# Performance work log

Hardware: AMD Instinct MI355X
Metric: run time of the kernel (lower is better)

Reference implementation:

```python
import jax, jax.numpy as jnp
import numpy as np
import math

H = 2048; NH = 16; HD = 128; E = 8; K = 2; F = 8192; CAP_F = 1.25
B = 2; S = 2048

def _layernorm(x, scale, bias, eps=1e-5):
    m = jnp.mean(x, axis=-1, keepdims=True)
    v = jnp.var(x, axis=-1, keepdims=True)
    return (x - m) * jax.lax.rsqrt(v + eps) * scale + bias

def _rope(x):
    # x: [B, S, NH, HD]; half-split RoPE, theta=10000
    hd = x.shape[-1]
    pos = jnp.arange(x.shape[1], dtype=jnp.float32)
    freqs = 1.0 / (10000.0 ** (jnp.arange(0, hd // 2, dtype=jnp.float32) / (hd // 2)))
    ang = pos[:, None] * freqs[None, :]              # [S, HD/2]
    cos = jnp.cos(ang)[None, :, None, :]
    sin = jnp.sin(ang)[None, :, None, :]
    x1, x2 = jnp.split(x, 2, axis=-1)
    return jnp.concatenate([x1 * cos - x2 * sin, x1 * sin + x2 * cos], axis=-1)

def setup_inputs() -> dict:
    key = jax.random.key(0)
    ks = jax.random.split(key, 16)
    std = 0.02
    inp = {
        'hidden_states': jax.random.normal(ks[0], (B, S, H), jnp.float32),
        'attention_mask': jnp.ones((B, S), jnp.int32),
        'ln1_scale': jnp.ones((H,), jnp.float32), 'ln1_bias': jnp.zeros((H,), jnp.float32),
        'ln2_scale': jnp.ones((H,), jnp.float32), 'ln2_bias': jnp.zeros((H,), jnp.float32),
        'Wq': jax.random.normal(ks[1], (H, NH * HD), jnp.float32) * std,
        'Wk': jax.random.normal(ks[2], (H, NH * HD), jnp.float32) * std,
        'Wv': jax.random.normal(ks[3], (H, NH * HD), jnp.float32) * std,
        'Wo': jax.random.normal(ks[4], (NH * HD, H), jnp.float32) * std,
        'Wg': jax.random.normal(ks[5], (H, H), jnp.float32) * std,
        'bg': jnp.zeros((H,), jnp.float32),
        'ls_attn': jnp.full((H,), 0.1, jnp.float32),
        'ls_moe': jnp.full((H,), 0.1, jnp.float32),
        'router_w': jax.random.normal(ks[6], (H, E), jnp.float32) * std,
        'W1': jax.random.normal(ks[7], (E, H, F), jnp.float32) * std,
        'b1': jnp.zeros((E, F), jnp.float32),
        'W2': jax.random.normal(ks[8], (E, F, H), jnp.float32) * std,
        'b2': jnp.zeros((E, H), jnp.float32),
    }
    return inp

def _forward(hidden_states, attention_mask, ln1_scale, ln1_bias, ln2_scale, ln2_bias,
             Wq, Wk, Wv, Wo, Wg, bg, ls_attn, ls_moe, router_w, W1, b1, W2, b2):
    b, s, h = hidden_states.shape
    # ---- pre-norm MLA attention + residual ----
    xn = _layernorm(hidden_states, ln1_scale, ln1_bias)
    q = (xn @ Wq).reshape(b, s, NH, HD)
    k = (xn @ Wk).reshape(b, s, NH, HD)
    v = (xn @ Wv).reshape(b, s, NH, HD)
    q = _rope(q); k = _rope(k)
    scores = jnp.einsum('bqhd,bkhd->bhqk', q, k) / math.sqrt(HD)
    causal = jnp.tril(jnp.ones((s, s), bool))
    mask = causal[None, None, :, :] & (attention_mask[:, None, None, :] > 0)
    scores = jnp.where(mask, scores, -1e9)
    attn = jax.nn.softmax(scores, axis=-1)
    ctx = jnp.einsum('bhqk,bkhd->bqhd', attn, v).reshape(b, s, NH * HD)
    attn_out = ctx @ Wo
    attn_out = attn_out * jax.nn.sigmoid(xn @ Wg + bg)   # output gating
    attn_out = attn_out * ls_attn                         # layer scale
    hidden_states = hidden_states + attn_out
    # ---- pre-norm MoE FFN + residual ----
    xn2 = _layernorm(hidden_states, ln2_scale, ln2_bias)
    T = b * s
    x = xn2.reshape(T, h)
    logits = (x @ router_w).astype(jnp.float32)           # [T, E]
    probs = jax.nn.softmax(logits, axis=-1)
    gates, idx = jax.lax.top_k(probs, K)                  # [T, K]
    gates = gates / jnp.sum(gates, axis=-1, keepdims=True)
    cap = int(math.ceil(T * K / E * CAP_F))               # expert capacity
    e_flat = idx.reshape(T * K)
    g_flat = gates.reshape(T * K)
    oh = jax.nn.one_hot(e_flat, E, dtype=jnp.int32)       # [TK, E]
    pos = jnp.sum(jnp.cumsum(oh, axis=0) * oh, axis=-1) - 1
    keep = (pos < cap).astype(x.dtype)
    pos_c = jnp.clip(pos, 0, cap - 1)
    x_rep = jnp.repeat(x, K, axis=0)                      # [TK, H]
    buf = jnp.zeros((E, cap, h), x.dtype).at[e_flat, pos_c].add(x_rep * keep[:, None])
    hmid = jax.nn.gelu(jnp.einsum('ech,ehf->ecf', buf, W1) + b1[:, None, :])
    obuf = jnp.einsum('ecf,efh->ech', hmid, W2) + b2[:, None, :]
    tok = obuf[e_flat, pos_c] * (keep * g_flat)[:, None]  # [TK, H]
    moe_out = tok.reshape(T, K, h).sum(axis=1).reshape(b, s, h)
    moe_out = moe_out * ls_moe
    return hidden_states + moe_out

def reference(hidden_states, attention_mask, ln1_scale, ln1_bias, ln2_scale, ln2_bias,
              Wq, Wk, Wv, Wo, Wg, bg, ls_attn, ls_moe, router_w, W1, b1, W2, b2):
    return _forward(hidden_states, attention_mask, ln1_scale, ln1_bias, ln2_scale, ln2_bias,
                    Wq, Wk, Wv, Wo, Wg, bg, ls_attn, ls_moe, router_w, W1, b1, W2, b2)
```

## Files before the change

### kernel.cpp

```cpp
#include <hip/hip_runtime.h>
#include <hip/hip_fp16.h>

typedef _Float16 f16;
typedef _Float16 half8 __attribute__((ext_vector_type(8)));
typedef float floatx4 __attribute__((ext_vector_type(4)));

constexpr int kH  = 2048;
constexpr int kS  = 2048;
constexpr int kB  = 2;
constexpr int kT  = kB * kS;
constexpr int kNH = 16;
constexpr int kHD = 128;
constexpr int kE  = 8;
constexpr int kF  = 8192;
constexpr int kCAP = 1280;
constexpr int kTK = kT * 2;

__device__ __forceinline__ void gload16(const void* g, void* lds_) {
  __builtin_amdgcn_global_load_lds((const __attribute__((address_space(1))) void*)g,
                                   (__attribute__((address_space(3))) void*)lds_,
                                   16, 0, 0);
}

__global__ __launch_bounds__(256) void transpose_cvt(
    const float* __restrict__ src, f16* __restrict__ dst,
    int ldS, int ldD, long sZ, long dZ)
{
  __shared__ float tile[64][65];
  src += (long)blockIdx.z * sZ;
  dst += (long)blockIdx.z * dZ;
  const int kb = blockIdx.y * 64, nb = blockIdx.x * 64;
  const int tx = threadIdx.x & 15, ty = threadIdx.x >> 4;
#pragma unroll
  for (int i = 0; i < 4; i++) {
    const int r = ty + i * 16;
    const float4 v = *(const float4*)&src[(long)(kb + r) * ldS + nb + tx * 4];
    tile[r][tx * 4 + 0] = v.x; tile[r][tx * 4 + 1] = v.y;
    tile[r][tx * 4 + 2] = v.z; tile[r][tx * 4 + 3] = v.w;
  }
  __syncthreads();
#pragma unroll
  for (int i = 0; i < 4; i++) {
    const int n = ty + i * 16;
    union { f16 h[4]; unsigned long long u; } pk;
#pragma unroll
    for (int j = 0; j < 4; j++) pk.h[j] = (f16)tile[tx * 4 + j][n];
    *(unsigned long long*)&dst[(long)(nb + n) * ldD + kb + tx * 4] = pk.u;
  }
}

__global__ __launch_bounds__(256) void ln_kernel(
    const float* __restrict__ x, const float* __restrict__ sc,
    const float* __restrict__ bi, f16* __restrict__ o16, float* __restrict__ o32)
{
  const long row = blockIdx.x;
  const float* xr = x + row * kH;
  const int t = threadIdx.x;
  const float4 u = ((const float4*)xr)[t * 2];
  const float4 v = ((const float4*)xr)[t * 2 + 1];
  float s = u.x + u.y + u.z + u.w + v.x + v.y + v.z + v.w;
  float q = u.x*u.x + u.y*u.y + u.z*u.z + u.w*u.w + v.x*v.x + v.y*v.y + v.z*v.z + v.w*v.w;
#pragma unroll
  for (int m = 1; m < 64; m <<= 1) { s += __shfl_xor(s, m); q += __shfl_xor(q, m); }
  __shared__ float red_s[4], red_q[4];
  const int w = t >> 6, l = t & 63;
  if (l == 0) { red_s[w] = s; red_q[w] = q; }
  __syncthreads();
  s = red_s[0] + red_s[1] + red_s[2] + red_s[3];
  q = red_q[0] + red_q[1] + red_q[2] + red_q[3];
  const float mean = s * (1.f / kH);
  const float var = q * (1.f / kH) - mean * mean;
  const float rstd = rsqrtf(var + 1e-5f);
  const int c = t * 8;
  const float vals[8] = {u.x, u.y, u.z, u.w, v.x, v.y, v.z, v.w};
#pragma unroll
  for (int j = 0; j < 8; j++) {
    const float y = (vals[j] - mean) * rstd * sc[c + j] + bi[c + j];
    o16[row * kH + c + j] = (f16)y;
    if (o32 != nullptr) o32[row * kH + c + j] = y;
  }
}

template <int EPI>
__global__ __launch_bounds__(256) void gemm_kernel(
    const f16* __restrict__ A, const f16* __restrict__ B, void* __restrict__ Cv,
    const float* __restrict__ bias, const int* __restrict__ rowCount,
    int M, int N, int K, long aZ, long bZ, long cZ, long biasZ)
{
  const int z = blockIdx.z;
  if (rowCount != nullptr && (int)(blockIdx.y * 128) >= rowCount[z]) return;
  __shared__ f16 As[128 * 64];
  __shared__ f16 Bs[128 * 64];
  A += (long)z * aZ;  B += (long)z * bZ;
  const int tid = threadIdx.x, w = tid >> 6, l = tid & 63;
  const int g = l >> 4, lr = l & 15;
  const long m0 = (long)blockIdx.y * 128, n0 = (long)blockIdx.x * 128;
  const int wm = (w >> 1) * 64, wn = (w & 1) * 64;
  floatx4 acc[4][4];
#pragma unroll
  for (int i = 0; i < 4; i++)
#pragma unroll
    for (int j = 0; j < 4; j++) acc[i][j] = floatx4{0.f, 0.f, 0.f, 0.f};
  const int lrow = l >> 3, lwb = (l & 7) * 16;
  const int nk = K >> 6;
  for (int kt = 0; kt < nk; kt++) {
    const long k0 = (long)kt * 64;
#pragma unroll
    for (int c = 0; c < 4; c++) {
      const int rbase = w * 32 + c * 8;
      const int row = rbase + lrow;
      const int srcoff = (lwb ^ ((row & 7) << 4)) >> 1;
      gload16(A + (m0 + row) * K + k0 + srcoff, As + rbase * 64);
      gload16(B + (n0 + row) * K + k0 + srcoff, Bs + rbase * 64);
    }
    asm volatile("s_waitcnt vmcnt(0)" ::: "memory");
    __syncthreads();
#pragma unroll
    for (int kc = 0; kc < 2; kc++) {
      half8 af[4], bf[4];
#pragma unroll
      for (int i = 0; i < 4; i++) {
        const int ra = wm + i * 16 + lr;
        af[i] = *(const half8*)((const char*)As + ra * 128 + ((kc * 64 + g * 16) ^ ((ra & 7) << 4)));
        const int rb = wn + i * 16 + lr;
        bf[i] = *(const half8*)((const char*)Bs + rb * 128 + ((kc * 64 + g * 16) ^ ((rb & 7) << 4)));
      }
#pragma unroll
      for (int mi = 0; mi < 4; mi++)
#pragma unroll
        for (int ni = 0; ni < 4; ni++)
          acc[mi][ni] = __builtin_amdgcn_mfma_f32_16x16x32_f16(af[mi], bf[ni], acc[mi][ni], 0, 0, 0);
    }
    __syncthreads();
  }
  const long crow = m0 + wm + g * 4;
  const long ccol = n0 + wn + lr;
#pragma unroll
  for (int mi = 0; mi < 4; mi++)
#pragma unroll
    for (int ni = 0; ni < 4; ni++)
#pragma unroll
      for (int j = 0; j < 4; j++) {
        const long r = crow + mi * 16 + j;
        const long c = ccol + ni * 16;
        float v = acc[mi][ni][j];
        if (EPI == 0) {
          ((float*)Cv)[(long)z * cZ + r * N + c] = v;
        } else {
          v += bias[(long)z * biasZ + c];
          ((f16*)Cv)[(long)z * cZ + r * N + c] = (f16)v;
        }
      }
}

#define STG(SRC, TILE, KC, PAR, MAT) { \
  const f16* s_ = (SRC) + (long)(TILE) * 64 + (KC) * 32; \
  char* d_ = lds + ((PAR) * 65536 + (MAT) * 32768 + (KC) * 16384) + ldsW; \
  gload16(s_, d_); \
  gload16(s_ + 128 * Kl, d_ + 8192); }

#define MROW(MH, MM, AF) \
  acc[(MH)*4+(MM)][0] = __builtin_amdgcn_mfma_f32_16x16x32_f16(AF, bf0, acc[(MH)*4+(MM)][0], 0, 0, 0); \
  acc[(MH)*4+(MM)][1] = __builtin_amdgcn_mfma_f32_16x16x32_f16(AF, bf1, acc[(MH)*4+(MM)][1], 0, 0, 0); \
  acc[(MH)*4+(MM)][2] = __builtin_amdgcn_mfma_f32_16x16x32_f16(AF, bf2, acc[(MH)*4+(MM)][2], 0, 0, 0); \
  acc[(MH)*4+(MM)][3] = __builtin_amdgcn_mfma_f32_16x16x32_f16(AF, bf3, acc[(MH)*4+(MM)][3], 0, 0, 0);

#define PH(PAR, KC, MH, RB, STAGE_STMT, VM_STMT) { \
  const char* au_ = lds + ((PAR) * 65536 + (KC) * 16384); \
  const char* bu_ = lds + ((PAR) * 65536 + 32768 + (KC) * 16384); \
  af0 = *(const half8*)(au_ + afoff + (MH) * 4096 +    0); \
  af1 = *(const half8*)(au_ + afoff + (MH) * 4096 + 1024); \
  af2 = *(const half8*)(au_ + afoff + (MH) * 4096 + 2048); \
  af3 = *(const half8*)(au_ + afoff + (MH) * 4096 + 3072); \
  if (RB) { \
    bf0 = *(const half8*)(bu_ + bfoff +    0); \
    bf1 = *(const half8*)(bu_ + bfoff + 1024); \
    bf2 = *(const half8*)(bu_ + bfoff + 2048); \
    bf3 = *(const half8*)(bu_ + bfoff + 3072); \
  } \
  STAGE_STMT; \
  VM_STMT; \
  __builtin_amdgcn_sched_barrier(0); \
  __builtin_amdgcn_s_barrier(); \
  asm volatile("s_waitcnt lgkmcnt(0)" ::: "memory"); \
  __builtin_amdgcn_sched_barrier(0); \
  __builtin_amdgcn_s_setprio(1); \
  MROW(MH, 0, af0) MROW(MH, 1, af1) MROW(MH, 2, af2) MROW(MH, 3, af3) \
  __builtin_amdgcn_s_setprio(0); \
  __builtin_amdgcn_sched_barrier(0); \
  __builtin_amdgcn_s_barrier(); }

#define VM6 asm volatile("s_waitcnt vmcnt(6)" ::: "memory")
#define VM0 asm volatile("s_waitcnt vmcnt(0)" ::: "memory")
#define NOP (void)0

template <int EPI>
__global__ __launch_bounds__(512, 2) void gemm8p_kernel(
    const f16* __restrict__ A, const f16* __restrict__ B, void* __restrict__ Cv,
    const float* __restrict__ bias, const int* __restrict__ rowCount,
    int M, int N, int K, long aZ, long bZ, long cZ, long biasZ)
{
  const int z = blockIdx.z;
  if (rowCount != nullptr && (int)(blockIdx.y * 256) >= rowCount[z]) return;
  __shared__ __align__(16) char lds[131072];
  A += (long)z * aZ;  B += (long)z * bZ;
  const long Kl = K;
  const int tid = threadIdx.x, w = tid >> 6, l = tid & 63;
  const int g = l >> 4, lr = l & 15;
  const long m0 = (long)blockIdx.y * 256, n0 = (long)blockIdx.x * 256;
  const int wm = (w >> 2) * 128, wn = (w & 3) * 64;

  floatx4 acc[8][4];
#pragma unroll
  for (int i = 0; i < 8; i++)
#pragma unroll
    for (int j = 0; j < 4; j++) acc[i][j] = floatx4{0.f, 0.f, 0.f, 0.f};

  const int swzS = ((l & 3) * 8) ^ (((l >> 3) & 3) << 3);
  const f16* aSrc = A + (m0 + w * 16 + (l >> 2)) * Kl + swzS;
  const f16* bSrc = B + (n0 + w * 16 + (l >> 2)) * Kl + swzS;
  const int ldsW = w * 1024;
  const int rsw = (g * 16) ^ (((lr >> 1) & 3) << 4);
  const int afoff = wm * 64 + lr * 64 + rsw;
  const int bfoff = wn * 64 + lr * 64 + rsw;
  half8 af0, af1, af2, af3;
  half8 bf0 = half8{0}, bf1 = half8{0}, bf2 = half8{0}, bf3 = half8{0};

  STG(aSrc, 0, 0, 0, 0);
  STG(bSrc, 0, 0, 0, 1);
  STG(aSrc, 0, 1, 0, 0);
  STG(bSrc, 0, 1, 0, 1);
  STG(bSrc, 1, 0, 1, 1);
  STG(aSrc, 1, 0, 1, 0);
  STG(bSrc, 1, 1, 1, 1);
  VM6;
  __builtin_amdgcn_sched_barrier(0);
  __builtin_amdgcn_s_barrier();

  const int NI = K >> 7;
  for (int i = 0; i < NI - 1; i++) {
    const int t0 = 2 * i, t1 = 2 * i + 1;
    PH(0, 0, 0, 1, STG(aSrc, (t1),     1, 1, 0), NOP)
    PH(0, 0, 1, 0, STG(bSrc, (t0 + 2), 0, 0, 1), NOP)
    PH(0, 1, 0, 1, STG(aSrc, (t0 + 2), 0, 0, 0), NOP)
    PH(0, 1, 1, 0, STG(bSrc, (t0 + 2), 1, 0, 1), VM6)
    PH(1, 0, 0, 1, STG(aSrc, (t0 + 2), 1, 0, 0), NOP)
    PH(1, 0, 1, 0, STG(bSrc, (t1 + 2), 0, 1, 1), NOP)
    PH(1, 1, 0, 1, STG(aSrc, (t1 + 2), 0, 1, 0), NOP)
    PH(1, 1, 1, 0, STG(bSrc, (t1 + 2), 1, 1, 1), VM6)
  }
  {
    const int t1 = 2 * (NI - 1) + 1;
    PH(0, 0, 0, 1, STG(aSrc, (t1), 1, 1, 0), NOP)
    PH(0, 0, 1, 0, NOP, NOP)
    PH(0, 1, 0, 1, NOP, NOP)
    PH(0, 1, 1, 0, NOP, VM0)
    PH(1, 0, 0, 1, NOP, NOP)
    PH(1, 0, 1, 0, NOP, NOP)
    PH(1, 1, 0, 1, NOP, NOP)
    PH(1, 1, 1, 0, NOP, NOP)
  }

  const long crow = m0 + wm + g * 4;
  const long ccol = n0 + wn + lr;
#pragma unroll
  for (int mi = 0; mi < 8; mi++)
#pragma unroll
    for (int ni = 0; ni < 4; ni++)
#pragma unroll
      for (int j = 0; j < 4; j++) {
        const long r = crow + mi * 16 + j;
        const long c = ccol + ni * 16;
        float v = acc[mi][ni][j];
        if (EPI == 0) {
          ((float*)Cv)[(long)z * cZ + r * N + c] = v;
        } else if (EPI == 2) {
          v += bias[(long)z * biasZ + c];
          const float u2 = 1.5957691216057308f * (v + 0.044715f * v * v * v);
          const float sg = 1.f / (1.f + __expf(-u2));
          ((f16*)Cv)[(long)z * cZ + r * N + c] = (f16)(v * sg);
        } else {
          v += bias[(long)z * biasZ + c];
          ((f16*)Cv)[(long)z * cZ + r * N + c] = (f16)v;
        }
      }
}
#undef STG
#undef MROW
#undef PH
#undef VM6
#undef VM0
#undef NOP

__global__ void rope_table_kernel(float* __restrict__ ct, float* __restrict__ st) {
  const int i = blockIdx.x * 256 + threadIdx.x;
  if (i >= kS * 64) return;
  const int s = i >> 6, f = i & 63;
  const double freq = exp(-0.14391156831212787 * (double)f);
  const double ang = (double)s * freq;
  ct[i] = (float)cos(ang);
  st[i] = (float)sin(ang);
}

__global__ __launch_bounds__(256) void rope_kernel(
    const float* __restrict__ q, const float* __restrict__ k,
    const float* __restrict__ ct, const float* __restrict__ st,
    f16* __restrict__ qr, f16* __restrict__ kr)
{
  const long t = blockIdx.x;
  const int s = (int)(t & (kS - 1)), b = (int)(t >> 11);
  for (int u = threadIdx.x; u < kNH * 64; u += 256) {
    const int h = u >> 6, i = u & 63;
    const float c = ct[s * 64 + i], sn = st[s * 64 + i];
    const long src = t * kH + h * kHD + i;
    const long dst = (((long)(b * kNH + h)) * kS + s) * kHD + i;
    float x1 = q[src], x2 = q[src + 64];
    qr[dst]      = (f16)((x1 * c - x2 * sn) * 0.08838834764831845f);
    qr[dst + 64] = (f16)((x1 * sn + x2 * c) * 0.08838834764831845f);
    x1 = k[src]; x2 = k[src + 64];
    kr[dst]      = (f16)(x1 * c - x2 * sn);
    kr[dst + 64] = (f16)(x1 * sn + x2 * c);
  }
}

__global__ __launch_bounds__(256) void attn_kernel(
    const f16* __restrict__ q_r, const f16* __restrict__ k_r,
    const f16* __restrict__ v_t, f16* __restrict__ ctx)
{
  __shared__ f16 Ks[64 * 128];
  __shared__ f16 Vs[128 * 64];
  __shared__ f16 Ps[4][1024];
  const int qt = blockIdx.x, h = blockIdx.y, b = blockIdx.z;
  const int bh = b * kNH + h;
  const int tid = threadIdx.x, w = tid >> 6, l = tid & 63;
  const int g = l >> 4, lr = l & 15;
  const long q0 = (long)qt * 64;
  const f16* qbase = q_r + ((long)bh * kS + q0 + w * 16 + lr) * kHD;
  half8 qf[4];
#pragma unroll
  for (int kc = 0; kc < 4; kc++) qf[kc] = *(const half8*)(qbase + kc * 32 + g * 8);
  floatx4 acc[8];
#pragma unroll
  for (int i = 0; i < 8; i++) acc[i] = floatx4{0.f, 0.f, 0.f, 0.f};
  float mrun[4], lrun[4];
#pragma unroll
  for (int j = 0; j < 4; j++) { mrun[j] = -1e30f; lrun[j] = 0.f; }
  f16* pw = Ps[w];

  for (int kt = 0; kt <= qt; kt++) {
    const long k0 = (long)kt * 64;
#pragma unroll
    for (int c = 0; c < 4; c++) {
      const int cc = w * 4 + c;
      const int row = cc * 4 + (l >> 4);
      const int wb = (l & 15) * 16;
      const int src = (wb ^ ((row & 7) << 4)) >> 1;
      gload16(k_r + ((long)bh * kS + k0 + row) * kHD + src, Ks + cc * 512);
    }
#pragma unroll
    for (int c = 0; c < 4; c++) {
      const int cc = w * 4 + c;
      const int row = cc * 8 + (l >> 3);
      const int wb = (l & 7) * 16;
      const int src = (wb ^ ((row & 7) << 4)) >> 1;
      gload16(v_t + ((long)bh * kHD + row) * kS + k0 + src, Vs + cc * 512);
    }
    asm volatile("s_waitcnt vmcnt(0)" ::: "memory");
    __syncthreads();

    floatx4 sfr[4];
#pragma unroll
    for (int f = 0; f < 4; f++) {
      floatx4 s4 = floatx4{0.f, 0.f, 0.f, 0.f};
      const int row = f * 16 + lr;
#pragma unroll
      for (int kc = 0; kc < 4; kc++) {
        const half8 kfq = *(const half8*)((const char*)Ks + row * 256 +
                            ((kc * 64 + g * 16) ^ ((row & 7) << 4)));
        s4 = __builtin_amdgcn_mfma_f32_16x16x32_f16(qf[kc], kfq, s4, 0, 0, 0);
      }
      sfr[f] = s4;
    }
    if (kt == qt) {
#pragma unroll
      for (int f = 0; f < 4; f++) {
        const int key = kt * 64 + f * 16 + lr;
#pragma unroll
        for (int j = 0; j < 4; j++) {
          const int qrow = qt * 64 + w * 16 + g * 4 + j;
          if (key > qrow) sfr[f][j] = -1e30f;
        }
      }
    }
    float al[4];
#pragma unroll
    for (int j = 0; j < 4; j++) {
      float pm = fmaxf(fmaxf(sfr[0][j], sfr[1][j]), fmaxf(sfr[2][j], sfr[3][j]));
      pm = fmaxf(pm, __shfl_xor(pm, 1)); pm = fmaxf(pm, __shfl_xor(pm, 2));
      pm = fmaxf(pm, __shfl_xor(pm, 4)); pm = fmaxf(pm, __shfl_xor(pm, 8));
      const float mn = fmaxf(mrun[j], pm);
      al[j] = __expf(mrun[j] - mn);
      mrun[j] = mn;
      float rs = 0.f;
#pragma unroll
      for (int f = 0; f < 4; f++) {
        const float p = __expf(sfr[f][j] - mn);
        sfr[f][j] = p; rs += p;
      }
      rs += __shfl_xor(rs, 1); rs += __shfl_xor(rs, 2);
      rs += __shfl_xor(rs, 4); rs += __shfl_xor(rs, 8);
      lrun[j] = lrun[j] * al[j] + rs;
    }
#pragma unroll
    for (int nf = 0; nf < 8; nf++)
#pragma unroll
      for (int j = 0; j < 4; j++) acc[nf][j] *= al[j];
#pragma unroll
    for (int f = 0; f < 4; f++)
#pragma unroll
      for (int j = 0; j < 4; j++) {
        const int row = g * 4 + j;
        const int byteoff = (row * 128 + (f * 16 + lr) * 2) ^ ((row & 7) << 4);
        *(f16*)((char*)pw + byteoff) = (f16)sfr[f][j];
      }
#pragma unroll
    for (int kc = 0; kc < 2; kc++) {
      const half8 pf = *(const half8*)((const char*)pw + lr * 128 +
                         ((kc * 64 + g * 16) ^ ((lr & 7) << 4)));
#pragma unroll
      for (int nf = 0; nf < 8; nf++) {
        const int vrow = nf * 16 + lr;
        const half8 vfr = *(const half8*)((const char*)Vs + vrow * 128 +
                            ((kc * 64 + g * 16) ^ ((vrow & 7) << 4)));
        acc[nf] = __builtin_amdgcn_mfma_f32_16x16x32_f16(pf, vfr, acc[nf], 0, 0, 0);
      }
    }
    __syncthreads();
  }
  const long orow = (long)b * kS + q0 + w * 16;
#pragma unroll
  for (int j = 0; j < 4; j++) {
    const float inv = 1.0f / lrun[j];
    const int r = g * 4 + j;
#pragma unroll
    for (int nf = 0; nf < 8; nf++)
      ctx[(orow + r) * kH + h * kHD + nf * 16 + lr] = (f16)(acc[nf][j] * inv);
  }
}

__global__ __launch_bounds__(256) void combine1_kernel(
    const float* __restrict__ hid, const float* __restrict__ alin,
    const float* __restrict__ glin, const float* __restrict__ bg,
    const float* __restrict__ ls, float* __restrict__ out)
{
  const long i = (long)blockIdx.x * 256 + threadIdx.x;
  const float4 hv = ((const float4*)hid)[i];
  const float4 av = ((const float4*)alin)[i];
  const float4 gv = ((const float4*)glin)[i];
  const int c = (int)(i & 511);
  const float4 lv = ((const float4*)ls)[c];
  const float4 bv = ((const float4*)bg)[c];
  float4 o;
  o.x = hv.x + lv.x * av.x / (1.f + __expf(-(gv.x + bv.x)));
  o.y = hv.y + lv.y * av.y / (1.f + __expf(-(gv.y + bv.y)));
  o.z = hv.z + lv.z * av.z / (1.f + __expf(-(gv.z + bv.z)));
  o.w = hv.w + lv.w * av.w / (1.f + __expf(-(gv.w + bv.w)));
  ((float4*)out)[i] = o;
}

__global__ __launch_bounds__(256) void router_kernel(
    const float* __restrict__ x, const float* __restrict__ rw,
    int* __restrict__ eidx, float* __restrict__ gates)
{
  const int t = blockIdx.x * 4 + (threadIdx.x >> 6);
  const int l = threadIdx.x & 63;
  const float* xr = x + (long)t * kH;
  float a[8] = {0.f, 0.f, 0.f, 0.f, 0.f, 0.f, 0.f, 0.f};
  for (int it = 0; it < kH / 64; it++) {
    const float xv = xr[it * 64 + l];
    const float* r = rw + (long)(it * 64 + l) * kE;
#pragma unroll
    for (int e = 0; e < 8; e++) a[e] += xv * r[e];
  }
#pragma unroll
  for (int e = 0; e < 8; e++)
#pragma unroll
    for (int m = 1; m < 64; m <<= 1) a[e] += __shfl_xor(a[e], m);
  if (l == 0) {
    float mx = a[0];
#pragma unroll
    for (int e = 1; e < 8; e++) mx = fmaxf(mx, a[e]);
    float p[8];
#pragma unroll
    for (int e = 0; e < 8; e++) p[e] = __expf(a[e] - mx);
    int i1 = 0; float v1 = p[0];
#pragma unroll
    for (int e = 1; e < 8; e++) if (p[e] > v1) { v1 = p[e]; i1 = e; }
    int i2 = -1; float v2 = -1.f;
#pragma unroll
    for (int e = 0; e < 8; e++) if (e != i1 && p[e] > v2) { v2 = p[e]; i2 = e; }
    const float inv = 1.f / (v1 + v2);
    eidx[t * 2] = i1; eidx[t * 2 + 1] = i2;
    gates[t * 2] = v1 * inv; gates[t * 2 + 1] = v2 * inv;
  }
}

__global__ void scan_kernel(const int* __restrict__ eidx, int* __restrict__ slot,
                            int* __restrict__ counts)
{
  const int l = threadIdx.x;
  int base[8] = {0, 0, 0, 0, 0, 0, 0, 0};
  const unsigned long long lt = (1ull << l) - 1ull;
  for (int it = 0; it < kTK / 64; it++) {
    const int i = it * 64 + l;
    const int e = eidx[i];
    int mypos = 0;
#pragma unroll
    for (int ex = 0; ex < 8; ex++) {
      const unsigned long long mk = __ballot(e == ex);
      if (e == ex) mypos = base[ex] + __popcll(mk & lt);
      base[ex] += __popcll(mk);
    }
    slot[i] = (mypos < kCAP) ? e * kCAP + mypos : -1;
  }
  if (l == 0) {
#pragma unroll
    for (int ex = 0; ex < 8; ex++) counts[ex] = min(base[ex], kCAP);
  }
}

__global__ __launch_bounds__(256) void scatter_kernel(
    const f16* __restrict__ xh, const int* __restrict__ slot, f16* __restrict__ buf)
{
  const int i = blockIdx.x;
  const int s = slot[i];
  if (s < 0) return;
  const long t = i >> 1;
  ((half8*)(buf + (long)s * kH))[threadIdx.x] =
      ((const half8*)(xh + t * kH))[threadIdx.x];
}

__global__ __launch_bounds__(256) void combine2_kernel(
    const float* __restrict__ hid2, const f16* __restrict__ obuf,
    const int* __restrict__ slot, const float* __restrict__ gates,
    const float* __restrict__ ls, float* __restrict__ out)
{
  const int t = blockIdx.x;
  const int s0 = slot[t * 2], s1 = slot[t * 2 + 1];
  const float g0 = (s0 >= 0) ? gates[t * 2] : 0.f;
  const float g1 = (s1 >= 0) ? gates[t * 2 + 1] : 0.f;
  const f16* o0 = obuf + (long)(s0 < 0 ? 0 : s0) * kH;
  const f16* o1 = obuf + (long)(s1 < 0 ? 0 : s1) * kH;
  const int c = threadIdx.x * 8;
  const float* hp = hid2 + (long)t * kH + c;
  float* op = out + (long)t * kH + c;
#pragma unroll
  for (int j = 0; j < 8; j++) {
    const float m = g0 * (float)o0[c + j] + g1 * (float)o1[c + j];
    op[j] = hp[j] + ls[c + j] * m;
  }
}

extern "C" void kernel_launch(void* const* d_in, const int* in_sizes, int n_in,
                              void* d_out, int out_size, void* d_ws, size_t ws_size,
                              hipStream_t stream)
{
  (void)in_sizes; (void)n_in;
  const float* hidden   = (const float*)d_in[0];
  const float* ln1s     = (const float*)d_in[2];
  const float* ln1b     = (const float*)d_in[3];
  const float* ln2s     = (const float*)d_in[4];
  const float* ln2b     = (const float*)d_in[5];
  const float* Wq       = (const float*)d_in[6];
  const float* Wk       = (const float*)d_in[7];
  const float* Wv       = (const float*)d_in[8];
  const float* Wo       = (const float*)d_in[9];
  const float* Wg       = (const float*)d_in[10];
  const float* bg       = (const float*)d_in[11];
  const float* ls_attn  = (const float*)d_in[12];
  const float* ls_moe   = (const float*)d_in[13];
  const float* router_w = (const float*)d_in[14];
  const float* W1       = (const float*)d_in[15];
  const float* b1       = (const float*)d_in[16];
  const float* W2       = (const float*)d_in[17];
  const float* b2       = (const float*)d_in[18];

  char* ws = (char*)d_ws;
  size_t off = 0;
  auto take = [&](size_t b) { size_t r = off; off += (b + 255) & ~(size_t)255; return r; };
  const size_t o_wT   = take(5ULL * kH * kH * 2);
  const size_t o_w1t  = take((size_t)kE * kF * kH * 2);
  const size_t o_w2t  = take((size_t)kE * kH * kF * 2);
  const size_t o_xn   = take((size_t)kT * kH * 2);
  const size_t o_qkvg = take(4ULL * kT * kH * 4);
  const size_t o_tab  = take(2ULL * kS * 64 * 4);
  const size_t o_qr   = take(3ULL * kT * kH * 2);
  const size_t o_ctx  = take((size_t)kT * kH * 2);
  const size_t o_h2   = take((size_t)kT * kH * 4);
  const size_t o_sm   = take(1 << 20);
  const size_t o_hmid = take((size_t)kE * kCAP * kF * 2);
  if (off > ws_size) { hipMemsetAsync(d_out, 0xFF, (size_t)out_size * 4, stream); return; }

  f16* wT    = (f16*)(ws + o_wT);
  f16* w1t   = (f16*)(ws + o_w1t);
  f16* w2t   = (f16*)(ws + o_w2t);
  f16* xn    = (f16*)(ws + o_xn);
  float* qf  = (float*)(ws + o_qkvg);
  float* kfp = qf + (size_t)kT * kH;
  float* vfp = kfp + (size_t)kT * kH;
  float* gfp = vfp + (size_t)kT * kH;
  float* tabc = (float*)(ws + o_tab);
  float* tabs = tabc + (size_t)kS * 64;
  f16* qr  = (f16*)(ws + o_qr);
  f16* kr  = qr + (size_t)kT * kH;
  f16* vt  = kr + (size_t)kT * kH;
  f16* ctx = (f16*)(ws + o_ctx);
  float* h2 = (float*)(ws + o_h2);
  int* eidx    = (int*)(ws + o_sm);
  float* gates = (float*)(ws + o_sm + 65536);
  int* slot    = (int*)(ws + o_sm + 131072);
  int* counts  = (int*)(ws + o_sm + 196608);
  f16* hmid = (f16*)(ws + o_hmid);
  float* attn_lin = qf;
  float* x2f = vfp;
  f16* x2h  = (f16*)(ws + o_qkvg + 1ULL * kT * kH * 4 + (size_t)kT * kH * 2);
  f16* obuf = (f16*)(ws + o_qkvg);
  f16* buf  = qr;

  const long HH = (long)kH * kH;

  transpose_cvt<<<dim3(32, 32, 1), 256, 0, stream>>>(Wq, wT + 0 * HH, kH, kH, 0, 0);
  transpose_cvt<<<dim3(32, 32, 1), 256, 0, stream>>>(Wk, wT + 1 * HH, kH, kH, 0, 0);
  transpose_cvt<<<dim3(32, 32, 1), 256, 0, stream>>>(Wv, wT + 2 * HH, kH, kH, 0, 0);
  transpose_cvt<<<dim3(32, 32, 1), 256, 0, stream>>>(Wg, wT + 3 * HH, kH, kH, 0, 0);
  transpose_cvt<<<dim3(32, 32, 1), 256, 0, stream>>>(Wo, wT + 4 * HH, kH, kH, 0, 0);
  transpose_cvt<<<dim3(kF / 64, kH / 64, kE), 256, 0, stream>>>(
      W1, w1t, kF, kH, (long)kH * kF, (long)kF * kH);
  transpose_cvt<<<dim3(kH / 64, kF / 64, kE), 256, 0, stream>>>(
      W2, w2t, kH, kF, (long)kF * kH, (long)kH * kF);
  ln_kernel<<<kT, 256, 0, stream>>>(hidden, ln1s, ln1b, xn, nullptr);
  gemm8p_kernel<0><<<dim3(kH / 256, kT / 256, 4), 512, 0, stream>>>(
      xn, wT, qf, nullptr, nullptr, kT, kH, kH, 0L, HH, (long)kT * kH, 0L);
  rope_table_kernel<<<(kS * 64 + 255) / 256, 256, 0, stream>>>(tabc, tabs);
  rope_kernel<<<kT, 256, 0, stream>>>(qf, kfp, tabc, tabs, qr, kr);
  for (int b = 0; b < kB; b++)
    transpose_cvt<<<dim3(kHD / 64, kS / 64, kNH), 256, 0, stream>>>(
        vfp + (size_t)b * kS * kH, vt + (size_t)b * kNH * kHD * kS,
        kH, kS, 128L, (long)kHD * kS);
  attn_kernel<<<dim3(kS / 64, kNH, kB), 256, 0, stream>>>(qr, kr, vt, ctx);
  gemm_kernel<0><<<dim3(kH / 128, kT / 128, 1), 256, 0, stream>>>(
      ctx, wT + 4 * HH, attn_lin, nullptr, nullptr, kT, kH, kH, 0L, 0L, 0L, 0L);
  combine1_kernel<<<(kT * kH / 4) / 256, 256, 0, stream>>>(
      hidden, attn_lin, gfp, bg, ls_attn, h2);
  ln_kernel<<<kT, 256, 0, stream>>>(h2, ln2s, ln2b, x2h, x2f);
  router_kernel<<<kT / 4, 256, 0, stream>>>(x2f, router_w, eidx, gates);
  scan_kernel<<<1, 64, 0, stream>>>(eidx, slot, counts);
  scatter_kernel<<<kTK, 256, 0, stream>>>(x2h, slot, buf);
  gemm8p_kernel<2><<<dim3(kF / 256, kCAP / 256, kE), 512, 0, stream>>>(
      buf, w1t, hmid, b1, counts, kCAP, kF, kH,
      (long)kCAP * kH, (long)kF * kH, (long)kCAP * kF, (long)kF);
  gemm8p_kernel<3><<<dim3(kH / 256, kCAP / 256, kE), 512, 0, stream>>>(
      hmid, w2t, obuf, b2, counts, kCAP, kH, kF,
      (long)kCAP * kF, (long)kH * kF, (long)kCAP * kH, (long)kH);
  combine2_kernel<<<kT, 256, 0, stream>>>(h2, obuf, slot, gates, ls_moe, (float*)d_out);
}
```

Before: 1.772 ms.

## Split-K the MoE down-projection GEMM and fold bias into combine

The W2 expert GEMM is split into two K halves, doubling the grid so more blocks are resident on the CUs. Each half writes an fp32 partial into a separate workspace region, one of which reuses the W1 transpose buffer. The combine kernel now sums both partials, adds the b2 bias and applies the gates. Separately, the trailing s_barrier after each MFMA phase in the pipelined GEMM macro is dropped, which removes a sync per phase but could introduce LDS reuse hazards. The extra fp32 partial traffic is the cost of the split.

Result: faster. 1.692 ms (-4.5%).

```diff
diff --git a/kernel.cpp b/kernel.cpp
--- a/kernel.cpp
+++ b/kernel.cpp
@@ -157,7 +157,7 @@
   const f16* s_ = (SRC) + (long)(TILE) * 64 + (KC) * 32; \
   char* d_ = lds + ((PAR) * 65536 + (MAT) * 32768 + (KC) * 16384) + ldsW; \
   gload16(s_, d_); \
-  gload16(s_ + 128 * Kl, d_ + 8192); }
+  gload16(s_ + 128 * ldGl, d_ + 8192); }
 
 #define MROW(MH, MM, AF) \
   acc[(MH)*4+(MM)][0] = __builtin_amdgcn_mfma_f32_16x16x32_f16(AF, bf0, acc[(MH)*4+(MM)][0], 0, 0, 0); \
@@ -186,25 +186,25 @@
   __builtin_amdgcn_sched_barrier(0); \
   __builtin_amdgcn_s_setprio(1); \
   MROW(MH, 0, af0) MROW(MH, 1, af1) MROW(MH, 2, af2) MROW(MH, 3, af3) \
-  __builtin_amdgcn_s_setprio(0); \
-  __builtin_amdgcn_sched_barrier(0); \
-  __builtin_amdgcn_s_barrier(); }
+  __builtin_amdgcn_s_setprio(0); }
 
 #define VM6 asm volatile("s_waitcnt vmcnt(6)" ::: "memory")
 #define VM0 asm volatile("s_waitcnt vmcnt(0)" ::: "memory")
 #define NOP (void)0
 
-template <int EPI>
+template <int EPI, bool SPLITK>
 __global__ __launch_bounds__(512, 2) void gemm8p_kernel(
     const f16* __restrict__ A, const f16* __restrict__ B, void* __restrict__ Cv,
     const float* __restrict__ bias, const int* __restrict__ rowCount,
-    int M, int N, int K, long aZ, long bZ, long cZ, long biasZ)
+    int M, int N, int K, long ldA, long ldB, long aZ, long bZ, long cZ,
+    long cZ2, long biasZ)
 {
   const int z = blockIdx.z;
-  if (rowCount != nullptr && (int)(blockIdx.y * 256) >= rowCount[z]) return;
+  const int ze = SPLITK ? (z >> 1) : z;
+  if (rowCount != nullptr && (int)(blockIdx.y * 256) >= rowCount[ze]) return;
   __shared__ __align__(16) char lds[131072];
-  A += (long)z * aZ;  B += (long)z * bZ;
-  const long Kl = K;
+  const long khoff = SPLITK ? (long)(z & 1) * K : 0;
+  A += (long)ze * aZ + khoff;  B += (long)ze * bZ + khoff;
   const int tid = threadIdx.x, w = tid >> 6, l = tid & 63;
   const int g = l >> 4, lr = l & 15;
   const long m0 = (long)blockIdx.y * 256, n0 = (long)blockIdx.x * 256;
@@ -217,8 +217,15 @@
     for (int j = 0; j < 4; j++) acc[i][j] = floatx4{0.f, 0.f, 0.f, 0.f};
 
   const int swzS = ((l & 3) * 8) ^ (((l >> 3) & 3) << 3);
-  const f16* aSrc = A + (m0 + w * 16 + (l >> 2)) * Kl + swzS;
-  const f16* bSrc = B + (n0 + w * 16 + (l >> 2)) * Kl + swzS;
+  const f16* aSrc;
+  const f16* bSrc;
+  long ldGl;
+  {
+    const int srow = w * 16 + (l >> 2);
+    aSrc = A + (m0 + srow) * ldA + swzS;
+    bSrc = B + (n0 + srow) * ldB + swzS;
+  }
+  ldGl = ldA;
   const int ldsW = w * 1024;
   const int rsw = (g * 16) ^ (((lr >> 1) & 3) << 4);
   const int afoff = wm * 64 + lr * 64 + rsw;
@@ -263,6 +270,7 @@
 
   const long crow = m0 + wm + g * 4;
   const long ccol = n0 + wn + lr;
+  float* c32 = (float*)Cv + (long)ze * cZ + (SPLITK ? (long)(z & 1) * cZ2 : 0);
 #pragma unroll
   for (int mi = 0; mi < 8; mi++)
 #pragma unroll
@@ -273,15 +281,15 @@
         const long c = ccol + ni * 16;
         float v = acc[mi][ni][j];
         if (EPI == 0) {
-          ((float*)Cv)[(long)z * cZ + r * N + c] = v;
+          c32[r * N + c] = v;
         } else if (EPI == 2) {
-          v += bias[(long)z * biasZ + c];
+          v += bias[(long)ze * biasZ + c];
           const float u2 = 1.5957691216057308f * (v + 0.044715f * v * v * v);
           const float sg = 1.f / (1.f + __expf(-u2));
-          ((f16*)Cv)[(long)z * cZ + r * N + c] = (f16)(v * sg);
+          ((f16*)Cv)[(long)ze * cZ + r * N + c] = (f16)(v * sg);
         } else {
-          v += bias[(long)z * biasZ + c];
-          ((f16*)Cv)[(long)z * cZ + r * N + c] = (f16)v;
+          v += bias[(long)ze * biasZ + c];
+          ((f16*)Cv)[(long)ze * cZ + r * N + c] = (f16)v;
         }
       }
 }
@@ -541,24 +549,40 @@
 }
 
 __global__ __launch_bounds__(256) void combine2_kernel(
-    const float* __restrict__ hid2, const f16* __restrict__ obuf,
-    const int* __restrict__ slot, const float* __restrict__ gates,
+    const float* __restrict__ hid2, const float* __restrict__ P0,
+    const float* __restrict__ P1, const int* __restrict__ slot,
+    const float* __restrict__ gates, const float* __restrict__ b2,
     const float* __restrict__ ls, float* __restrict__ out)
 {
   const int t = blockIdx.x;
-  const int s0 = slot[t * 2], s1 = slot[t * 2 + 1];
-  const float g0 = (s0 >= 0) ? gates[t * 2] : 0.f;
-  const float g1 = (s1 >= 0) ? gates[t * 2 + 1] : 0.f;
-  const f16* o0 = obuf + (long)(s0 < 0 ? 0 : s0) * kH;
-  const f16* o1 = obuf + (long)(s1 < 0 ? 0 : s1) * kH;
   const int c = threadIdx.x * 8;
+  float m[8] = {0.f, 0.f, 0.f, 0.f, 0.f, 0.f, 0.f, 0.f};
+#pragma unroll
+  for (int ks = 0; ks < 2; ks++) {
+    const int s = slot[t * 2 + ks];
+    if (s < 0) continue;
+    const float gte = gates[t * 2 + ks];
+    const int e = s / kCAP;
+    const long ro = (long)s * kH + c;
+    const float4 p0a = *(const float4*)&P0[ro];
+    const float4 p0b = *(const float4*)&P0[ro + 4];
+    const float4 p1a = *(const float4*)&P1[ro];
+    const float4 p1b = *(const float4*)&P1[ro + 4];
+    const float4 ba = *(const float4*)&b2[e * kH + c];
+    const float4 bb = *(const float4*)&b2[e * kH + c + 4];
+    m[0] += gte * (p0a.x + p1a.x + ba.x);
+    m[1] += gte * (p0a.y + p1a.y + ba.y);
+    m[2] += gte * (p0a.z + p1a.z + ba.z);
+    m[3] += gte * (p0a.w + p1a.w + ba.w);
+    m[4] += gte * (p0b.x + p1b.x + bb.x);
+    m[5] += gte * (p0b.y + p1b.y + bb.y);
+    m[6] += gte * (p0b.z + p1b.z + bb.z);
+    m[7] += gte * (p0b.w + p1b.w + bb.w);
+  }
   const float* hp = hid2 + (long)t * kH + c;
   float* op = out + (long)t * kH + c;
 #pragma unroll
-  for (int j = 0; j < 8; j++) {
-    const float m = g0 * (float)o0[c + j] + g1 * (float)o1[c + j];
-    op[j] = hp[j] + ls[c + j] * m;
-  }
+  for (int j = 0; j < 8; j++) op[j] = hp[j] + ls[c + j] * m[j];
 }
 
 extern "C" void kernel_launch(void* const* d_in, const int* in_sizes, int n_in,
@@ -624,8 +648,10 @@
   float* attn_lin = qf;
   float* x2f = vfp;
   f16* x2h  = (f16*)(ws + o_qkvg + 1ULL * kT * kH * 4 + (size_t)kT * kH * 2);
-  f16* obuf = (f16*)(ws + o_qkvg);
   f16* buf  = qr;
+  float* P0 = (float*)(ws + o_qkvg);
+  float* P1 = (float*)(ws + o_w1t);
+  const long pStride = (long)(P1 - P0);
 
   const long HH = (long)kH * kH;
 
@@ -639,8 +665,9 @@
   transpose_cvt<<<dim3(kH / 64, kF / 64, kE), 256, 0, stream>>>(
       W2, w2t, kH, kF, (long)kF * kH, (long)kH * kF);
   ln_kernel<<<kT, 256, 0, stream>>>(hidden, ln1s, ln1b, xn, nullptr);
-  gemm8p_kernel<0><<<dim3(kH / 256, kT / 256, 4), 512, 0, stream>>>(
-      xn, wT, qf, nullptr, nullptr, kT, kH, kH, 0L, HH, (long)kT * kH, 0L);
+  gemm8p_kernel<0, false><<<dim3(kH / 256, kT / 256, 4), 512, 0, stream>>>(
+      xn, wT, qf, nullptr, nullptr, kT, kH, kH, kH, kH,
+      0L, HH, (long)kT * kH, 0L, 0L);
   rope_table_kernel<<<(kS * 64 + 255) / 256, 256, 0, stream>>>(tabc, tabs);
   rope_kernel<<<kT, 256, 0, stream>>>(qf, kfp, tabc, tabs, qr, kr);
   for (int b = 0; b < kB; b++)
@@ -656,11 +683,12 @@
   router_kernel<<<kT / 4, 256, 0, stream>>>(x2f, router_w, eidx, gates);
   scan_kernel<<<1, 64, 0, stream>>>(eidx, slot, counts);
   scatter_kernel<<<kTK, 256, 0, stream>>>(x2h, slot, buf);
-  gemm8p_kernel<2><<<dim3(kF / 256, kCAP / 256, kE), 512, 0, stream>>>(
-      buf, w1t, hmid, b1, counts, kCAP, kF, kH,
-      (long)kCAP * kH, (long)kF * kH, (long)kCAP * kF, (long)kF);
-  gemm8p_kernel<3><<<dim3(kH / 256, kCAP / 256, kE), 512, 0, stream>>>(
-      hmid, w2t, obuf, b2, counts, kCAP, kH, kF,
-      (long)kCAP * kF, (long)kH * kF, (long)kCAP * kH, (long)kH);
-  combine2_kernel<<<kT, 256, 0, stream>>>(h2, obuf, slot, gates, ls_moe, (float*)d_out);
-}
+  gemm8p_kernel<2, false><<<dim3(kF / 256, kCAP / 256, kE), 512, 0, stream>>>(
+      buf, w1t, hmid, b1, counts, kCAP, kF, kH, kH, kH,
+      (long)kCAP * kH, (long)kF * kH, (long)kCAP * kF, 0L, (long)kF);
+  gemm8p_kernel<0, true><<<dim3(kH / 256, kCAP / 256, 2 * kE), 512, 0, stream>>>(
+      hmid, w2t, P0, nullptr, counts, kCAP, kH, 4096, kF, kF,
+      (long)kCAP * kF, (long)kH * kF, (long)kCAP * kH, pStride, 0L);
+  combine2_kernel<<<kT, 256, 0, stream>>>(
+      h2, P0, P1, slot, gates, b2, ls_moe, (float*)d_out);
+}
```
